# Kernel optimization log

Hardware: AMD Instinct MI355X
Metric: run time of the kernel (lower is better)

The kernel has to match this reference:

```python
import jax, jax.numpy as jnp
import numpy as np

INPUT_DIM = 4096
EPS = 1e-8


def _ste_bit(v):
    # {0,1} bit with straight-through gradient
    b = (v >= 0).astype(v.dtype)
    return v + jax.lax.stop_gradient(b - v)


def _ste_sign(v):
    # {-1,+1} sign with straight-through gradient
    s = jnp.where(v >= 0, 1.0, -1.0).astype(v.dtype)
    return v + jax.lax.stop_gradient(s - v)


def setup_inputs() -> dict:
    key = jax.random.key(0)
    k1, k2, k3 = jax.random.split(key, 3)
    x = jax.random.normal(k1, (8192, 4096), dtype=jnp.float32)
    mag_bits = jax.random.normal(k2, (3, 4096, 4096), dtype=jnp.float32)  # [nbBits-1, in, out]
    sign_bit = jax.random.normal(k3, (4096, 4096), dtype=jnp.float32)     # [in, out]
    return {"x": x, "mag_bits": mag_bits, "sign_bit": sign_bit}


def reference(x, mag_bits, sign_bit):
    nbits = mag_bits.shape[0]
    # bit-plane composition: W_mag = sum_k bit_k * 2^-(k+1)
    powers = (2.0 ** -(jnp.arange(1, nbits + 1))).astype(mag_bits.dtype)  # [K]
    bits = _ste_bit(mag_bits)                                             # [K, in, out]
    w = _ste_sign(sign_bit) * jnp.einsum('kio,k->io', bits, powers)       # [in, out]
    # rescale so std(W) matches kaiming std (original does this via a detached
    # numpy round-trip, so no gradient flows through alpha)
    std_target = np.sqrt(2.0 / INPUT_DIM).astype(np.float32)
    alpha = jax.lax.stop_gradient(std_target / (jnp.std(w) + EPS))
    w = w * alpha
    # F.linear(x, W.T) == x @ W
    return x @ w
```

## Files before the change

kernel.cpp:

```cpp
#include <hip/hip_runtime.h>
#include <hip/hip_bf16.h>
#include <stdint.h>

#define K_DIM 4096
#define M_DIM 8192
#define N_DIM 4096

typedef short bf16x8 __attribute__((ext_vector_type(8)));
typedef float f32x4  __attribute__((ext_vector_type(4)));

__device__ __forceinline__ uint16_t f2bf(float f) {
  uint32_t u = __float_as_uint(f);
  u += 0x7fffu + ((u >> 16) & 1u);
  return (uint16_t)(u >> 16);
}

__device__ __forceinline__ float wval(float b0, float b1, float b2, float sg) {
  float mg = (b0 >= 0.f ? 0.5f : 0.f) + (b1 >= 0.f ? 0.25f : 0.f) + (b2 >= 0.f ? 0.125f : 0.f);
  return (sg >= 0.f) ? mg : -mg;
}

__device__ __forceinline__ void gload16(const void* g, void* l) {
  typedef __attribute__((address_space(1))) const uint32_t gu32;
  typedef __attribute__((address_space(3))) uint32_t lu32;
  __builtin_amdgcn_global_load_lds((gu32*)g, (lu32*)l, 16, 0, 0);
}

__global__ __launch_bounds__(256) void build_wt(
    const float* __restrict__ mag, const float* __restrict__ sgn,
    uint16_t* __restrict__ wt, float* __restrict__ psum, float* __restrict__ psumsq)
{
  __shared__ float wl[64][65];
  __shared__ float parts[8];
  const int tid = threadIdx.x;
  const int lr = tid >> 4;
  const int lc = tid & 15;
  const int i0 = blockIdx.y * 64;
  const int o0 = blockIdx.x * 64;
  const float* m0 = mag;
  const float* m1 = mag + (size_t)K_DIM * N_DIM;
  const float* m2 = mag + 2 * (size_t)K_DIM * N_DIM;

  float s = 0.f, s2 = 0.f;
  #pragma unroll
  for (int rg = 0; rg < 4; ++rg) {
    int il = rg * 16 + lr;
    size_t base = (size_t)(i0 + il) * N_DIM + o0 + lc * 4;
    float4 a = *(const float4*)(m0 + base);
    float4 b = *(const float4*)(m1 + base);
    float4 c = *(const float4*)(m2 + base);
    float4 g = *(const float4*)(sgn + base);
    float w0 = wval(a.x, b.x, c.x, g.x);
    float w1 = wval(a.y, b.y, c.y, g.y);
    float w2 = wval(a.z, b.z, c.z, g.z);
    float w3 = wval(a.w, b.w, c.w, g.w);
    wl[il][lc * 4 + 0] = w0;
    wl[il][lc * 4 + 1] = w1;
    wl[il][lc * 4 + 2] = w2;
    wl[il][lc * 4 + 3] = w3;
    s  += w0 + w1 + w2 + w3;
    s2 += w0 * w0 + w1 * w1 + w2 * w2 + w3 * w3;
  }
  #pragma unroll
  for (int off = 32; off > 0; off >>= 1) {
    s  += __shfl_down(s,  off);
    s2 += __shfl_down(s2, off);
  }
  if ((tid & 63) == 0) { parts[tid >> 6] = s; parts[4 + (tid >> 6)] = s2; }
  __syncthreads();
  if (tid == 0) {
    int bid = blockIdx.y * gridDim.x + blockIdx.x;
    psum[bid]   = parts[0] + parts[1] + parts[2] + parts[3];
    psumsq[bid] = parts[4] + parts[5] + parts[6] + parts[7];
  }
  #pragma unroll
  for (int rg = 0; rg < 4; ++rg) {
    int ol = rg * 16 + lr;
    int il = lc * 4;
    ushort4 v;
    v.x = f2bf(wl[il + 0][ol]);
    v.y = f2bf(wl[il + 1][ol]);
    v.z = f2bf(wl[il + 2][ol]);
    v.w = f2bf(wl[il + 3][ol]);
    *(ushort4*)(wt + (size_t)(o0 + ol) * K_DIM + i0 + il) = v;
  }
}

__global__ __launch_bounds__(256) void cvt_x(const float* __restrict__ x,
                                             uint16_t* __restrict__ xb, int n8)
{
  int idx = blockIdx.x * blockDim.x + threadIdx.x;
  int stride = gridDim.x * blockDim.x;
  for (; idx < n8; idx += stride) {
    float4 v0 = ((const float4*)x)[2 * idx];
    float4 v1 = ((const float4*)x)[2 * idx + 1];
    ushort4 r0, r1;
    r0.x = f2bf(v0.x); r0.y = f2bf(v0.y); r0.z = f2bf(v0.z); r0.w = f2bf(v0.w);
    r1.x = f2bf(v1.x); r1.y = f2bf(v1.y); r1.z = f2bf(v1.z); r1.w = f2bf(v1.w);
    ((ushort4*)xb)[2 * idx]     = r0;
    ((ushort4*)xb)[2 * idx + 1] = r1;
  }
}

__global__ __launch_bounds__(256) void calc_alpha(const float* __restrict__ psum,
                                                  const float* __restrict__ psumsq,
                                                  float* __restrict__ alpha, int nparts)
{
  __shared__ float ls[256], lq[256];
  int tid = threadIdx.x;
  float s = 0.f, q = 0.f;
  for (int i = tid; i < nparts; i += 256) { s += psum[i]; q += psumsq[i]; }
  ls[tid] = s; lq[tid] = q;
  __syncthreads();
  for (int off = 128; off > 0; off >>= 1) {
    if (tid < off) { ls[tid] += ls[tid + off]; lq[tid] += lq[tid + off]; }
    __syncthreads();
  }
  if (tid == 0) {
    const float n = 16777216.f;
    float mean = ls[0] / n;
    float var  = lq[0] / n - mean * mean;
    var = var < 0.f ? 0.f : var;
    float stdv = sqrtf(var);
    alpha[0] = 0.022097086912079608f / (stdv + 1e-8f);
  }
}

__global__ __launch_bounds__(512, 2) void gemm_bf16_v7(
    const uint16_t* __restrict__ xb, const uint16_t* __restrict__ wt,
    const float* __restrict__ alphap, float* __restrict__ out)
{
  __shared__ __align__(16) unsigned char sA[2][256 * 128];
  __shared__ __align__(16) unsigned char sB[2][256 * 128];

  const int tid  = threadIdx.x;
  const int lane = tid & 63;
  const int wv   = tid >> 6;
  const int wm   = wv >> 2;
  const int wn   = wv & 3;

  const int bid = blockIdx.x;
  const int xcd = bid & 7;
  const int c   = bid >> 3;
  const int bm  = (xcd >> 1) * 8 + (c >> 3);
  const int bn  = (xcd & 1) * 8 + (c & 7);

  const size_t rowA0 = (size_t)bm * 256;
  const size_t rowB0 = (size_t)bn * 256;

  f32x4 acc[8][4] = {};

  const int l15   = lane & 15;
  const int src_x = ((lane & 7) ^ (lane >> 3)) << 4;
  const int cb0   = (((lane >> 4) << 4)) ^ ((lane & 7) << 4);
  const int cb1   = (64 | ((lane >> 4) << 4)) ^ ((lane & 7) << 4);

#define STA(cc_, mh, h, kt)                                                         \
  gload16((const char*)xb + (((rowA0 + (h) * 128 + (mh) * 64 + wv * 8 + (lane >> 3)) \
              * (size_t)K_DIM + (size_t)(kt) * 64) << 1) + src_x,                   \
          &sA[cc_][((mh) * 128 + (h) * 64 + wv * 8) * 128])
#define STB(cc_, bh, h, kt)                                                         \
  gload16((const char*)wt + (((rowB0 + (2 * (h) + (wv >> 2)) * 64 + (bh) * 32       \
              + (wv & 3) * 8 + (lane >> 3)) * (size_t)K_DIM + (size_t)(kt) * 64) << 1) + src_x, \
          &sB[cc_][((bh) * 128 + (h) * 64 + wv * 8) * 128])
#define STAGE_A(cc_, mh, kt) do { STA(cc_, mh, 0, kt); STA(cc_, mh, 1, kt); } while (0)
#define STAGE_B(cc_, bh, kt) do { STB(cc_, bh, 0, kt); STB(cc_, bh, 1, kt); } while (0)

#define LDA8(Ap, mh, dst) do { _Pragma("unroll")                                    \
  for (int m = 0; m < 4; ++m) {                                                     \
    const unsigned char* rp = (Ap) + (size_t)((mh) * 128 + wm * 64 + m * 16 + l15) * 128; \
    dst[2 * m]     = *(const bf16x8*)(rp + cb0);                                    \
    dst[2 * m + 1] = *(const bf16x8*)(rp + cb1); } } while (0)
#define LDB4(Bp, bh, dst) do { _Pragma("unroll")                                    \
  for (int n = 0; n < 2; ++n) {                                                     \
    const unsigned char* rp = (Bp) + (size_t)((bh) * 128 + wn * 32 + n * 16 + l15) * 128; \
    dst[2 * n]     = *(const bf16x8*)(rp + cb0);                                    \
    dst[2 * n + 1] = *(const bf16x8*)(rp + cb1); } } while (0)

#define MMQ(AF, BF, mh, bh) do {                                                    \
  __builtin_amdgcn_s_setprio(1);                                                    \
  _Pragma("unroll") for (int m = 0; m < 4; ++m)                                     \
    _Pragma("unroll") for (int n = 0; n < 2; ++n) {                                 \
      acc[(mh)*4+m][(bh)*2+n] = __builtin_amdgcn_mfma_f32_16x16x32_bf16(            \
          AF[2*m],   BF[2*n],   acc[(mh)*4+m][(bh)*2+n], 0, 0, 0);                  \
      acc[(mh)*4+m][(bh)*2+n] = __builtin_amdgcn_mfma_f32_16x16x32_bf16(            \
          AF[2*m+1], BF[2*n+1], acc[(mh)*4+m][(bh)*2+n], 0, 0, 0); }                \
  __builtin_amdgcn_s_setprio(0); } while (0)

#define SCHED0   __builtin_amdgcn_sched_barrier(0)
#define LGKM0    do { asm volatile("s_waitcnt lgkmcnt(0)" ::: "memory"); SCHED0; } while (0)
#define WAITV(N) do { asm volatile("s_waitcnt vmcnt(" #N ")"   ::: "memory"); SCHED0; } while (0)
#define BAR      do { asm volatile("s_barrier" ::: "memory"); SCHED0; } while (0)

  bf16x8 A0f[8], A1f[8], B0f[4], B1f[4];

  STAGE_A(0, 0, 0); STAGE_B(0, 0, 0); STAGE_B(0, 1, 0); STAGE_A(0, 1, 0);
  STAGE_A(1, 0, 1); STAGE_B(1, 0, 1);
  WAITV(4);
  BAR;
  LDA8(sA[0], 0, A0f); LDB4(sB[0], 0, B0f); SCHED0;

  #pragma unroll 1
  for (int u = 0; u < 64; ++u) {
    const int cc = u & 1, oc = cc ^ 1;
    const unsigned char* Acur = sA[cc];
    const unsigned char* Bcur = sB[cc];
    const unsigned char* Aoth = sA[oc];
    const unsigned char* Both = sB[oc];
    const int k1 = (u + 1 < 64) ? (u + 1) : 63;
    const int k2 = (u + 2 < 64) ? (u + 2) : 63;

    STAGE_B(oc, 1, k1);
    BAR; LGKM0;
    MMQ(A0f, B0f, 0, 0);
    LDB4(Bcur, 1, B1f); SCHED0;

    STAGE_A(oc, 1, k1);
    BAR; LGKM0;
    MMQ(A0f, B1f, 0, 1);
    LDA8(Acur, 1, A1f); SCHED0;

    STAGE_A(cc, 0, k2);
    BAR; LGKM0;
    MMQ(A1f, B0f, 1, 0);

    STAGE_B(cc, 0, k2);
    WAITV(4);
    BAR; LGKM0;
    MMQ(A1f, B1f, 1, 1);
    LDA8(Aoth, 0, A0f); LDB4(Both, 0, B0f); SCHED0;
  }

#undef STA
#undef STB
#undef STAGE_A
#undef STAGE_B
#undef LDA8
#undef LDB4
#undef MMQ
#undef SCHED0
#undef LGKM0
#undef WAITV
#undef BAR

  const float alpha = alphap[0];
  const int ccol  = bn * 256 + wn * 64 + l15;
  const int crow0 = bm * 256 + wm * 128 + ((lane >> 4) << 2);
  #pragma unroll
  for (int am = 0; am < 8; ++am)
    #pragma unroll
    for (int an = 0; an < 4; ++an)
      #pragma unroll
      for (int r = 0; r < 4; ++r)
        out[(size_t)(crow0 + am * 16 + r) * N_DIM + ccol + an * 16] = acc[am][an][r] * alpha;
}

extern "C" void kernel_launch(void* const* d_in, const int* in_sizes, int n_in,
                              void* d_out, int out_size, void* d_ws, size_t ws_size,
                              hipStream_t stream) {
  const float* x   = (const float*)d_in[0];
  const float* mag = (const float*)d_in[1];
  const float* sgn = (const float*)d_in[2];
  float* out = (float*)d_out;

  char* ws = (char*)d_ws;
  float* alpha    = (float*)ws;
  float* psum     = (float*)(ws + 256);
  float* psumsq   = (float*)(ws + 256 + 16384);
  uint16_t* wt    = (uint16_t*)(ws + 256 + 32768);
  uint16_t* xb    = (uint16_t*)(ws + 256 + 32768 + 33554432ull);
  size_t needed = 256 + 32768 + 33554432ull + 67108864ull;
  if (ws_size < needed) return;

  build_wt<<<dim3(64, 64), 256, 0, stream>>>(mag, sgn, wt, psum, psumsq);
  cvt_x<<<dim3(2048), 256, 0, stream>>>(x, xb, (M_DIM * K_DIM) / 8);
  calc_alpha<<<dim3(1), 256, 0, stream>>>(psum, psumsq, alpha, 4096);
  gemm_bf16_v7<<<dim3(512), 512, 0, stream>>>(xb, wt, alpha, out);
}
```

Measured before the change: 329.7 us.

## Restructure GEMM main loop to prefetch next fragments before each MFMA quadrant

The bf16 GEMM main loop is unrolled by two k-tiles. Each LDS fragment load is now issued before the MFMA block that precedes its use, rather than after, so the read latency overlaps with matrix math. The staging order changes, one more B half is prefetched in the prologue, and extra barriers are added to protect buffer reuse. The MFMA order is also reordered k-outer so consecutive MFMAs are independent. This adds barriers and register pressure and makes the shared-memory hazards more delicate.

Measured after the change: 480.8 us. +45.8%, slower.

```diff
diff --git a/kernel.cpp b/kernel.cpp
--- a/kernel.cpp
+++ b/kernel.cpp
@@ -126,7 +126,7 @@
   }
 }
 
-__global__ __launch_bounds__(512, 2) void gemm_bf16_v7(
+__global__ __launch_bounds__(512, 2) void gemm_bf16_ra(
     const uint16_t* __restrict__ xb, const uint16_t* __restrict__ wt,
     const float* __restrict__ alphap, float* __restrict__ out)
 {
@@ -179,12 +179,11 @@
 
 #define MMQ(AF, BF, mh, bh) do {                                                    \
   __builtin_amdgcn_s_setprio(1);                                                    \
-  _Pragma("unroll") for (int m = 0; m < 4; ++m)                                     \
-    _Pragma("unroll") for (int n = 0; n < 2; ++n) {                                 \
-      acc[(mh)*4+m][(bh)*2+n] = __builtin_amdgcn_mfma_f32_16x16x32_bf16(            \
-          AF[2*m],   BF[2*n],   acc[(mh)*4+m][(bh)*2+n], 0, 0, 0);                  \
-      acc[(mh)*4+m][(bh)*2+n] = __builtin_amdgcn_mfma_f32_16x16x32_bf16(            \
-          AF[2*m+1], BF[2*n+1], acc[(mh)*4+m][(bh)*2+n], 0, 0, 0); }                \
+  _Pragma("unroll") for (int kk = 0; kk < 2; ++kk)                                  \
+    _Pragma("unroll") for (int m = 0; m < 4; ++m)                                   \
+      _Pragma("unroll") for (int n = 0; n < 2; ++n)                                 \
+        acc[(mh)*4+m][(bh)*2+n] = __builtin_amdgcn_mfma_f32_16x16x32_bf16(          \
+            AF[2*m+kk], BF[2*n+kk], acc[(mh)*4+m][(bh)*2+n], 0, 0, 0);              \
   __builtin_amdgcn_s_setprio(0); } while (0)
 
 #define SCHED0   __builtin_amdgcn_sched_barrier(0)
@@ -195,40 +194,63 @@
   bf16x8 A0f[8], A1f[8], B0f[4], B1f[4];
 
   STAGE_A(0, 0, 0); STAGE_B(0, 0, 0); STAGE_B(0, 1, 0); STAGE_A(0, 1, 0);
-  STAGE_A(1, 0, 1); STAGE_B(1, 0, 1);
-  WAITV(4);
-  BAR;
+  STAGE_A(1, 0, 1); STAGE_B(1, 0, 1); STAGE_B(1, 1, 1);
+  WAITV(0); BAR;
   LDA8(sA[0], 0, A0f); LDB4(sB[0], 0, B0f); SCHED0;
 
   #pragma unroll 1
-  for (int u = 0; u < 64; ++u) {
-    const int cc = u & 1, oc = cc ^ 1;
-    const unsigned char* Acur = sA[cc];
-    const unsigned char* Bcur = sB[cc];
-    const unsigned char* Aoth = sA[oc];
-    const unsigned char* Both = sB[oc];
-    const int k1 = (u + 1 < 64) ? (u + 1) : 63;
-    const int k2 = (u + 2 < 64) ? (u + 2) : 63;
-
-    STAGE_B(oc, 1, k1);
-    BAR; LGKM0;
+  for (int t = 0; t < 32; ++t) {
+    const unsigned char* Ab0 = sA[0];
+    const unsigned char* Bb0 = sB[0];
+    const unsigned char* Ab1 = sA[1];
+    const unsigned char* Bb1 = sB[1];
+    const int k1 = 2 * t + 1;
+    const int k2 = (2 * t + 2 < 64) ? 2 * t + 2 : 63;
+    const int k3 = (2 * t + 3 < 64) ? 2 * t + 3 : 63;
+
+    STAGE_A(1, 1, k1);
+    BAR; LGKM0;
+    LDB4(Bb0, 1, B1f); SCHED0;
     MMQ(A0f, B0f, 0, 0);
-    LDB4(Bcur, 1, B1f); SCHED0;
-
-    STAGE_A(oc, 1, k1);
-    BAR; LGKM0;
+    BAR;
+    STAGE_A(0, 0, k2);
+    BAR; LGKM0;
+    LDA8(Ab0, 1, A1f); SCHED0;
     MMQ(A0f, B1f, 0, 1);
-    LDA8(Acur, 1, A1f); SCHED0;
-
-    STAGE_A(cc, 0, k2);
-    BAR; LGKM0;
+    BAR;
+    STAGE_B(0, 0, k2);
+    BAR; LGKM0;
+    LDA8(Ab1, 0, A0f); SCHED0;
     MMQ(A1f, B0f, 1, 0);
-
-    STAGE_B(cc, 0, k2);
+    BAR;
+    STAGE_B(0, 1, k2);
     WAITV(4);
     BAR; LGKM0;
+    LDB4(Bb1, 0, B0f); SCHED0;
     MMQ(A1f, B1f, 1, 1);
-    LDA8(Aoth, 0, A0f); LDB4(Both, 0, B0f); SCHED0;
+    BAR;
+
+    STAGE_A(0, 1, k2);
+    BAR; LGKM0;
+    LDB4(Bb1, 1, B1f); SCHED0;
+    MMQ(A0f, B0f, 0, 0);
+    BAR;
+    STAGE_A(1, 0, k3);
+    BAR; LGKM0;
+    LDA8(Ab1, 1, A1f); SCHED0;
+    MMQ(A0f, B1f, 0, 1);
+    BAR;
+    STAGE_B(1, 0, k3);
+    BAR; LGKM0;
+    LDA8(Ab0, 0, A0f); SCHED0;
+    MMQ(A1f, B0f, 1, 0);
+    BAR;
+    STAGE_B(1, 1, k3);
+    WAITV(4);
+    BAR; LGKM0;
+    LDB4(Bb0, 0, B0f); SCHED0;
+    MMQ(A1f, B1f, 1, 1);
+    BAR;
   }
 
 #undef STA
@@ -275,5 +297,5 @@
   build_wt<<<dim3(64, 64), 256, 0, stream>>>(mag, sgn, wt, psum, psumsq);
   cvt_x<<<dim3(2048), 256, 0, stream>>>(x, xb, (M_DIM * K_DIM) / 8);
   calc_alpha<<<dim3(1), 256, 0, stream>>>(psum, psumsq, alpha, 4096);
-  gemm_bf16_v7<<<dim3(512), 512, 0, stream>>>(xb, wt, alpha, out);
-}
+  gemm_bf16_ra<<<dim3(512), 512, 0, stream>>>(xb, wt, alpha, out);
+}
```
